# Optimization experiments

Measured on AMD Instinct MI355X. Metric: run time of the kernel, lower is better.

## Reference

```python
import jax, jax.numpy as jnp
import numpy as np

IN_SIZE = 1024
CLASSES = 7
N = 50000
LN_EPS = 1e-5


def _chain(x, w, b, g, beta):
    # Linear -> (Dropout=identity at eval) -> LayerNorm -> GELU(exact erf)
    h = x @ w.T + b
    mu = jnp.mean(h, axis=-1, keepdims=True)
    var = jnp.var(h, axis=-1, keepdims=True)
    h = (h - mu) / jnp.sqrt(var + LN_EPS) * g + beta
    return jax.nn.gelu(h, approximate=False)


def setup_inputs() -> dict:
    key = jax.random.key(0)
    ks = jax.random.split(key, 16)
    d = IN_SIZE
    std = 1.0 / np.sqrt(d)
    inp = {
        "features": jax.random.normal(ks[0], (N, d), jnp.float32),
        "c": jax.random.normal(ks[1], (N, CLASSES), jnp.float32),
        "key_w": jax.random.uniform(ks[2], (d, d), jnp.float32, -std, std),
        "key_b": jax.random.uniform(ks[3], (d,), jnp.float32, -std, std),
        "key_g": jnp.ones((d,), jnp.float32),
        "key_beta": jnp.zeros((d,), jnp.float32),
        "query_w": jax.random.uniform(ks[4], (d, d), jnp.float32, -std, std),
        "query_b": jax.random.uniform(ks[5], (d,), jnp.float32, -std, std),
        "query_g": jnp.ones((d,), jnp.float32),
        "query_beta": jnp.zeros((d,), jnp.float32),
        "value_w": jax.random.uniform(ks[6], (d, d), jnp.float32, -std, std),
        "value_b": jax.random.uniform(ks[7], (d,), jnp.float32, -std, std),
        "value_g": jnp.ones((d,), jnp.float32),
        "value_beta": jnp.zeros((d,), jnp.float32),
        "head_w": jax.random.uniform(ks[8], (CLASSES, CLASSES, d), jnp.float32, -1.0 / np.sqrt(CLASSES * d), 1.0 / np.sqrt(CLASSES * d)),
        "head_b": jax.random.uniform(ks[9], (CLASSES,), jnp.float32, -1.0 / np.sqrt(CLASSES * d), 1.0 / np.sqrt(CLASSES * d)),
    }
    return inp


def reference(features, c, key_w, key_b, key_g, key_beta,
              query_w, query_b, query_g, query_beta,
              value_w, value_b, value_g, value_beta,
              head_w, head_b):
    K = _chain(features, key_w, key_b, key_g, key_beta)          # [N, d]
    V = _chain(K, value_w, value_b, value_g, value_beta)         # [N, d]
    Q = _chain(K, query_w, query_b, query_g, query_beta)         # [N, d]
    # critical (top-scoring) instance per class
    top_idx = jnp.argmax(c, axis=0)                              # [classes]
    m_feats = K[top_idx]                                         # [classes, d]
    q_max = _chain(m_feats, query_w, query_b, query_g, query_beta)  # [classes, d]
    A = Q @ q_max.T                                              # [N, classes]
    A = jax.nn.softmax(A / jnp.sqrt(jnp.float32(Q.shape[1])), axis=0)
    B = A.T @ V                                                  # [classes, d]
    # Conv1d(classes, classes, kernel_size=d) on [1, classes, d] -> full contraction
    C = jnp.einsum('ik,oik->o', B, head_w) + head_b              # [classes]
    C = C.reshape(1, -1)
    return (C, A, B.reshape(1, CLASSES, -1))
```

## Files before the change

kernel.cpp:

```cpp
#include <hip/hip_runtime.h>


typedef unsigned short u16;
typedef __attribute__((ext_vector_type(8))) short          bf16x8;
typedef __attribute__((ext_vector_type(8))) unsigned short u16x8;
typedef __attribute__((ext_vector_type(4))) unsigned short u16x4;
typedef __attribute__((ext_vector_type(4))) float          f32x4;

#define DDIM  1024
#define NROWS 50000
#define MP    50048
#define NCLS  7
#define MPD4  12512

__device__ __forceinline__ u16 f2bf(float f) {
  unsigned u = __float_as_uint(f);
  u = (u + 0x7FFFu + ((u >> 16) & 1u)) >> 16;
  return (u16)u;
}
__device__ __forceinline__ float bf2f(u16 h) {
  return __uint_as_float(((unsigned)h) << 16);
}
__device__ __forceinline__ float gelu(float x) {
  return 0.5f * x * (1.0f + erff(x * 0.70710678118654752f));
}

__device__ __forceinline__ void load16_lds(const u16* g, u16* l) {
  __builtin_amdgcn_global_load_lds(
      (const __attribute__((address_space(1))) unsigned int*)(const void*)g,
      (__attribute__((address_space(3))) unsigned int*)(void*)l, 16, 0, 0);
}

__global__ __launch_bounds__(256) void k_convw(const float* __restrict__ kw,
                                               const float* __restrict__ vw,
                                               const float* __restrict__ qw,
                                               u16* __restrict__ Wk,
                                               u16* __restrict__ Wvq) {
  const int w = blockIdx.x >> 7;
  const int b = blockIdx.x & 127;
  const float* src = (w == 0) ? kw : (w == 1) ? vw : qw;
  u16* dst = (w == 0) ? Wk : (Wvq + (size_t)(w - 1) * DDIM * DDIM);
  for (int i = b * 256 + threadIdx.x; i < DDIM * DDIM / 8; i += 128 * 256) {
    const float4* p = (const float4*)(src + (size_t)i * 8);
    float4 f0 = p[0], f1 = p[1];
    u16x8 o;
    o[0] = f2bf(f0.x); o[1] = f2bf(f0.y); o[2] = f2bf(f0.z); o[3] = f2bf(f0.w);
    o[4] = f2bf(f1.x); o[5] = f2bf(f1.y); o[6] = f2bf(f1.z); o[7] = f2bf(f1.w);
    *(u16x8*)(dst + (size_t)i * 8) = o;
  }
}

template<int AFP32>
__global__ __launch_bounds__(256) void k_gemm(const float* __restrict__ Af,
                                              const u16* __restrict__ Ab,
                                              const u16* __restrict__ B,
                                              u16* __restrict__ C,
                                              int lnn, int ldc) {
  __shared__ __align__(16) u16 As[128 * 32];
  __shared__ __align__(16) u16 Bs[128 * 32];
  const int tid  = threadIdx.x;
  const int lane = tid & 63;
  const int cpx = gridDim.x >> 3;
  const int v   = (blockIdx.x & 7) * cpx + (blockIdx.x >> 3);
  const int m0 = (v >> lnn) * 128;
  const int n0 = (v & ((1 << lnn) - 1)) * 128;
  const int wid = tid >> 6;
  const int wr = (wid >> 1) * 64;
  const int wc = (wid & 1) * 64;

  const int rA = tid >> 2;
  const int slotl = tid & 3;
  const int swz = (rA >> 1) & 3;
  const int cA = ((slotl ^ swz) << 3);
  const u16* Bp0 = B + (size_t)(n0 + rA) * DDIM + cA;
  const u16* Bp1 = Bp0 + (size_t)64 * DDIM;
  const u16* Ap0 = nullptr; const u16* Ap1 = nullptr;
  const float* Fp0 = nullptr; const float* Fp1 = nullptr;
  bool av0 = false, av1 = false;
  if (AFP32) {
    av0 = (m0 + rA) < NROWS;
    av1 = (m0 + rA + 64) < NROWS;
    Fp0 = Af + (size_t)(m0 + rA) * DDIM + slotl * 8;
    Fp1 = Fp0 + (size_t)64 * DDIM;
  } else {
    Ap0 = Ab + (size_t)(m0 + rA) * DDIM + cA;
    Ap1 = Ap0 + (size_t)64 * DDIM;
  }
  const int wbase = wid * 64;
  u16* AsD0 = &As[(wbase)       * 8];
  u16* AsD1 = &As[(wbase + 256) * 8];
  u16* BsD0 = &Bs[(wbase)       * 8];
  u16* BsD1 = &Bs[(wbase + 256) * 8];
  u16* AsW0 = &As[rA * 32 + (cA ^ 0)];
  u16* AsW1 = &As[(rA + 64) * 32 + cA];

  f32x4 acc[4][4] = {};
  const int fr = lane & 15;
  const int T  = lane >> 4;

  for (int k0 = 0; k0 < DDIM; k0 += 32) {
    float4 fa0, fb0, fa1, fb1;
    if (AFP32) {
      if (av0) { fa0 = *(const float4*)(Fp0 + k0); fb0 = *(const float4*)(Fp0 + k0 + 4); }
      if (av1) { fa1 = *(const float4*)(Fp1 + k0); fb1 = *(const float4*)(Fp1 + k0 + 4); }
    }
    __syncthreads();
    if (AFP32) {
      u16x8 o0 = {0,0,0,0,0,0,0,0}, o1 = {0,0,0,0,0,0,0,0};
      if (av0) {
        o0[0]=f2bf(fa0.x); o0[1]=f2bf(fa0.y); o0[2]=f2bf(fa0.z); o0[3]=f2bf(fa0.w);
        o0[4]=f2bf(fb0.x); o0[5]=f2bf(fb0.y); o0[6]=f2bf(fb0.z); o0[7]=f2bf(fb0.w);
      }
      if (av1) {
        o1[0]=f2bf(fa1.x); o1[1]=f2bf(fa1.y); o1[2]=f2bf(fa1.z); o1[3]=f2bf(fa1.w);
        o1[4]=f2bf(fb1.x); o1[5]=f2bf(fb1.y); o1[6]=f2bf(fb1.z); o1[7]=f2bf(fb1.w);
      }
      *(u16x8*)AsW0 = o0;
      *(u16x8*)AsW1 = o1;
    } else {
      load16_lds(Ap0 + k0, AsD0);
      load16_lds(Ap1 + k0, AsD1);
    }
    load16_lds(Bp0 + k0, BsD0);
    load16_lds(Bp1 + k0, BsD1);
    __syncthreads();
    bf16x8 a[4], b[4];
#pragma unroll
    for (int i = 0; i < 4; ++i) {
      const int R = wr + i * 16 + fr;
      a[i] = *(const bf16x8*)&As[R * 32 + ((T ^ ((R >> 1) & 3)) << 3)];
    }
#pragma unroll
    for (int j = 0; j < 4; ++j) {
      const int R = wc + j * 16 + fr;
      b[j] = *(const bf16x8*)&Bs[R * 32 + ((T ^ ((R >> 1) & 3)) << 3)];
    }
#pragma unroll
    for (int i = 0; i < 4; ++i)
#pragma unroll
      for (int j = 0; j < 4; ++j)
        acc[i][j] = __builtin_amdgcn_mfma_f32_16x16x32_bf16(a[i], b[j], acc[i][j], 0, 0, 0);
  }

  const int orow = (lane >> 4) * 4;
  const int ocol = lane & 15;
#pragma unroll
  for (int i = 0; i < 4; ++i)
#pragma unroll
    for (int j = 0; j < 4; ++j) {
      const size_t base = (size_t)(m0 + wr + i * 16 + orow) * ldc + (n0 + wc + j * 16 + ocol);
#pragma unroll
      for (int r = 0; r < 4; ++r)
        C[base + (size_t)r * ldc] = f2bf(acc[i][j][r]);
    }
}

__global__ __launch_bounds__(256) void k_ln_k(const u16* __restrict__ h,
                                              const float* __restrict__ bias,
                                              const float* __restrict__ g,
                                              const float* __restrict__ beta,
                                              u16* __restrict__ out) {
  const int lane = threadIdx.x & 63;
  const int row = blockIdx.x * 4 + (threadIdx.x >> 6);
  const int c0 = lane * 8;
  u16x8* op0 = (u16x8*)(out + (size_t)row * DDIM + c0);
  u16x8* op1 = (u16x8*)(out + (size_t)row * DDIM + 512 + c0);
  if (row >= NROWS) {
    u16x8 z = {0, 0, 0, 0, 0, 0, 0, 0};
    *op0 = z; *op1 = z;
    return;
  }
  u16x8 h0 = *(const u16x8*)(h + (size_t)row * DDIM + c0);
  u16x8 h1 = *(const u16x8*)(h + (size_t)row * DDIM + 512 + c0);
  float4 a0 = *(const float4*)(bias + c0), a1 = *(const float4*)(bias + c0 + 4);
  float4 a2 = *(const float4*)(bias + 512 + c0), a3 = *(const float4*)(bias + 512 + c0 + 4);
  const float ba[8] = {a0.x, a0.y, a0.z, a0.w, a1.x, a1.y, a1.z, a1.w};
  const float bb[8] = {a2.x, a2.y, a2.z, a2.w, a3.x, a3.y, a3.z, a3.w};
  float v0[8], v1[8];
  float s1 = 0.f, s2 = 0.f;
#pragma unroll
  for (int e = 0; e < 8; ++e) {
    v0[e] = bf2f(h0[e]) + ba[e];
    v1[e] = bf2f(h1[e]) + bb[e];
    s1 += v0[e] + v1[e];
    s2 += v0[e] * v0[e] + v1[e] * v1[e];
  }
#pragma unroll
  for (int m = 1; m < 64; m <<= 1) {
    s1 += __shfl_xor(s1, m, 64);
    s2 += __shfl_xor(s2, m, 64);
  }
  const float mu = s1 * (1.0f / 1024.0f);
  const float var = s2 * (1.0f / 1024.0f) - mu * mu;
  const float rs = rsqrtf(var + 1e-5f);
  float4 g0 = *(const float4*)(g + c0), g1 = *(const float4*)(g + c0 + 4);
  float4 g2 = *(const float4*)(g + 512 + c0), g3 = *(const float4*)(g + 512 + c0 + 4);
  float4 t0 = *(const float4*)(beta + c0), t1 = *(const float4*)(beta + c0 + 4);
  float4 t2 = *(const float4*)(beta + 512 + c0), t3 = *(const float4*)(beta + 512 + c0 + 4);
  const float ga[8] = {g0.x, g0.y, g0.z, g0.w, g1.x, g1.y, g1.z, g1.w};
  const float gb[8] = {g2.x, g2.y, g2.z, g2.w, g3.x, g3.y, g3.z, g3.w};
  const float ta[8] = {t0.x, t0.y, t0.z, t0.w, t1.x, t1.y, t1.z, t1.w};
  const float tb[8] = {t2.x, t2.y, t2.z, t2.w, t3.x, t3.y, t3.z, t3.w};
  u16x8 o0, o1;
#pragma unroll
  for (int e = 0; e < 8; ++e) {
    o0[e] = f2bf(gelu((v0[e] - mu) * rs * ga[e] + ta[e]));
    o1[e] = f2bf(gelu((v1[e] - mu) * rs * gb[e] + tb[e]));
  }
  *op0 = o0; *op1 = o1;
}

__global__ __launch_bounds__(64) void k_qmax2(const float* __restrict__ argv,
                                              const int* __restrict__ argi,
                                              const u16* __restrict__ hvq,
                                              const float* __restrict__ qb,
                                              const float* __restrict__ qg,
                                              const float* __restrict__ qbeta,
                                              u16* __restrict__ qm) {
  const int j = blockIdx.x;
  const int lane = threadIdx.x;
  float bv = -3.4e38f; int bi = 0x7fffffff;
  for (int p = lane; p < 128; p += 64) {
    const float v = argv[p * NCLS + j];
    const int   i = argi[p * NCLS + j];
    if (v > bv || (v == bv && i < bi)) { bv = v; bi = i; }
  }
#pragma unroll
  for (int m = 1; m < 64; m <<= 1) {
    const float ov = __shfl_xor(bv, m, 64);
    const int   oi = __shfl_xor(bi, m, 64);
    if (ov > bv || (ov == bv && oi < bi)) { bv = ov; bi = oi; }
  }
  const int row = bi;
  const int c0 = lane * 8;
  const u16* hp = hvq + (size_t)row * 2048 + DDIM;
  u16x8 h0 = *(const u16x8*)(hp + c0);
  u16x8 h1 = *(const u16x8*)(hp + 512 + c0);
  float v0[8], v1[8];
  float s1 = 0.f, s2 = 0.f;
#pragma unroll
  for (int e = 0; e < 8; ++e) {
    v0[e] = bf2f(h0[e]) + qb[c0 + e];
    v1[e] = bf2f(h1[e]) + qb[512 + c0 + e];
    s1 += v0[e] + v1[e];
    s2 += v0[e] * v0[e] + v1[e] * v1[e];
  }
#pragma unroll
  for (int m = 1; m < 64; m <<= 1) {
    s1 += __shfl_xor(s1, m, 64);
    s2 += __shfl_xor(s2, m, 64);
  }
  const float mu = s1 * (1.0f / 1024.0f);
  const float var = s2 * (1.0f / 1024.0f) - mu * mu;
  const float rs = rsqrtf(var + 1e-5f);
  u16x8 o0, o1;
#pragma unroll
  for (int e = 0; e < 8; ++e) {
    o0[e] = f2bf(gelu((v0[e] - mu) * rs * qg[c0 + e] + qbeta[c0 + e]));
    o1[e] = f2bf(gelu((v1[e] - mu) * rs * qg[512 + c0 + e] + qbeta[512 + c0 + e]));
  }
  *(u16x8*)(qm + (size_t)j * DDIM + c0) = o0;
  *(u16x8*)(qm + (size_t)j * DDIM + 512 + c0) = o1;
}

__global__ __launch_bounds__(256) void k_ln_vq(const u16* __restrict__ h,
                                               const float* __restrict__ v_b,
                                               const float* __restrict__ v_g,
                                               const float* __restrict__ v_beta,
                                               const float* __restrict__ q_b,
                                               const float* __restrict__ q_g,
                                               const float* __restrict__ q_beta,
                                               const u16* __restrict__ qm,
                                               u16* __restrict__ V,
                                               float* __restrict__ logits) {
  __shared__ __align__(16) u16 sqm[NCLS * DDIM];
  const int tid = threadIdx.x;
  const int lane = tid & 63;
  const int half = (blockIdx.x >= MPD4) ? 1 : 0;
  const int rb = half ? (blockIdx.x - MPD4) : blockIdx.x;
  const int row = rb * 4 + (tid >> 6);
  if (half) {
    for (int i = tid; i < NCLS * DDIM / 8; i += 256)
      *(u16x8*)&sqm[i * 8] = *(const u16x8*)&qm[i * 8];
    __syncthreads();
  }
  if (row >= NROWS) return;
  const float* bias = half ? q_b : v_b;
  const float* gain = half ? q_g : v_g;
  const float* bet  = half ? q_beta : v_beta;
  const int c0 = lane * 8;
  const u16* hp = h + (size_t)row * 2048 + (size_t)half * DDIM;
  u16x8 h0 = *(const u16x8*)(hp + c0);
  u16x8 h1 = *(const u16x8*)(hp + 512 + c0);
  float4 a0 = *(const float4*)(bias + c0), a1 = *(const float4*)(bias + c0 + 4);
  float4 a2 = *(const float4*)(bias + 512 + c0), a3 = *(const float4*)(bias + 512 + c0 + 4);
  const float ba[8] = {a0.x, a0.y, a0.z, a0.w, a1.x, a1.y, a1.z, a1.w};
  const float bb[8] = {a2.x, a2.y, a2.z, a2.w, a3.x, a3.y, a3.z, a3.w};
  float v0[8], v1[8];
  float s1 = 0.f, s2 = 0.f;
#pragma unroll
  for (int e = 0; e < 8; ++e) {
    v0[e] = bf2f(h0[e]) + ba[e];
    v1[e] = bf2f(h1[e]) + bb[e];
    s1 += v0[e] + v1[e];
    s2 += v0[e] * v0[e] + v1[e] * v1[e];
  }
#pragma unroll
  for (int m = 1; m < 64; m <<= 1) {
    s1 += __shfl_xor(s1, m, 64);
    s2 += __shfl_xor(s2, m, 64);
  }
  const float mu = s1 * (1.0f / 1024.0f);
  const float var = s2 * (1.0f / 1024.0f) - mu * mu;
  const float rs = rsqrtf(var + 1e-5f);
  float4 g0 = *(const float4*)(gain + c0), g1 = *(const float4*)(gain + c0 + 4);
  float4 g2 = *(const float4*)(gain + 512 + c0), g3 = *(const float4*)(gain + 512 + c0 + 4);
  float4 t0 = *(const float4*)(bet + c0), t1 = *(const float4*)(bet + c0 + 4);
  float4 t2 = *(const float4*)(bet + 512 + c0), t3 = *(const float4*)(bet + 512 + c0 + 4);
  const float ga[8] = {g0.x, g0.y, g0.z, g0.w, g1.x, g1.y, g1.z, g1.w};
  const float gb[8] = {g2.x, g2.y, g2.z, g2.w, g3.x, g3.y, g3.z, g3.w};
  const float ta[8] = {t0.x, t0.y, t0.z, t0.w, t1.x, t1.y, t1.z, t1.w};
  const float tb[8] = {t2.x, t2.y, t2.z, t2.w, t3.x, t3.y, t3.z, t3.w};
  float y0[8], y1[8];
#pragma unroll
  for (int e = 0; e < 8; ++e) {
    y0[e] = gelu((v0[e] - mu) * rs * ga[e] + ta[e]);
    y1[e] = gelu((v1[e] - mu) * rs * gb[e] + tb[e]);
  }
  if (half == 0) {
    u16x8 o0, o1;
#pragma unroll
    for (int e = 0; e < 8; ++e) { o0[e] = f2bf(y0[e]); o1[e] = f2bf(y1[e]); }
    *(u16x8*)(V + (size_t)row * DDIM + c0) = o0;
    *(u16x8*)(V + (size_t)row * DDIM + 512 + c0) = o1;
  } else {
#pragma unroll
    for (int j = 0; j < NCLS; ++j) {
      u16x8 m0 = *(const u16x8*)&sqm[j * DDIM + c0];
      u16x8 m1 = *(const u16x8*)&sqm[j * DDIM + 512 + c0];
      float p = 0.f;
#pragma unroll
      for (int e = 0; e < 8; ++e) p += y0[e] * bf2f(m0[e]) + y1[e] * bf2f(m1[e]);
#pragma unroll
      for (int m = 1; m < 64; m <<= 1) p += __shfl_xor(p, m, 64);
      if (lane == 0) logits[(size_t)row * NCLS + j] = p * 0.03125f;
    }
  }
}

__global__ __launch_bounds__(256) void k_arg1(const float* __restrict__ c,
                                              float* __restrict__ pv,
                                              int* __restrict__ pi) {
  __shared__ float sv[256 * NCLS];
  __shared__ int   si[256 * NCLS];
  const int t = threadIdx.x;
  float bv[NCLS]; int bi[NCLS];
#pragma unroll
  for (int j = 0; j < NCLS; ++j) { bv[j] = -3.4e38f; bi[j] = 0x7fffffff; }
  for (int n = blockIdx.x * 256 + t; n < NROWS; n += 128 * 256) {
#pragma unroll
    for (int j = 0; j < NCLS; ++j) {
      const float v = c[(size_t)n * NCLS + j];
      if (v > bv[j]) { bv[j] = v; bi[j] = n; }
    }
  }
#pragma unroll
  for (int j = 0; j < NCLS; ++j) { sv[t * NCLS + j] = bv[j]; si[t * NCLS + j] = bi[j]; }
  __syncthreads();
  for (int s = 128; s > 0; s >>= 1) {
    if (t < s) {
#pragma unroll
      for (int j = 0; j < NCLS; ++j) {
        const float v2 = sv[(t + s) * NCLS + j]; const int i2 = si[(t + s) * NCLS + j];
        const float v1 = sv[t * NCLS + j];       const int i1 = si[t * NCLS + j];
        if (v2 > v1 || (v2 == v1 && i2 < i1)) { sv[t * NCLS + j] = v2; si[t * NCLS + j] = i2; }
      }
    }
    __syncthreads();
  }
  if (t < NCLS) { pv[blockIdx.x * NCLS + t] = sv[t]; pi[blockIdx.x * NCLS + t] = si[t]; }
}

__global__ __launch_bounds__(256) void k_softpart(const float* __restrict__ logits,
                                                  float* __restrict__ Pm,
                                                  float* __restrict__ Ps) {
  __shared__ float sm[256 * NCLS];
  const int t = threadIdx.x;
  float m[NCLS];
#pragma unroll
  for (int j = 0; j < NCLS; ++j) m[j] = -3.4e38f;
  for (int n = blockIdx.x * 256 + t; n < NROWS; n += 128 * 256)
#pragma unroll
    for (int j = 0; j < NCLS; ++j) m[j] = fmaxf(m[j], logits[(size_t)n * NCLS + j]);
#pragma unroll
  for (int j = 0; j < NCLS; ++j) sm[t * NCLS + j] = m[j];
  __syncthreads();
  for (int s = 128; s > 0; s >>= 1) {
    if (t < s)
#pragma unroll
      for (int j = 0; j < NCLS; ++j)
        sm[t * NCLS + j] = fmaxf(sm[t * NCLS + j], sm[(t + s) * NCLS + j]);
    __syncthreads();
  }
  float mloc[NCLS];
#pragma unroll
  for (int j = 0; j < NCLS; ++j) mloc[j] = sm[j];
  __syncthreads();
  float s[NCLS];
#pragma unroll
  for (int j = 0; j < NCLS; ++j) s[j] = 0.f;
  for (int n = blockIdx.x * 256 + t; n < NROWS; n += 128 * 256)
#pragma unroll
    for (int j = 0; j < NCLS; ++j) s[j] += expf(logits[(size_t)n * NCLS + j] - mloc[j]);
#pragma unroll
  for (int j = 0; j < NCLS; ++j) sm[t * NCLS + j] = s[j];
  __syncthreads();
  for (int st = 128; st > 0; st >>= 1) {
    if (t < st)
#pragma unroll
      for (int j = 0; j < NCLS; ++j) sm[t * NCLS + j] += sm[(t + st) * NCLS + j];
    __syncthreads();
  }
  if (t < NCLS) { Pm[blockIdx.x * NCLS + t] = mloc[t]; Ps[blockIdx.x * NCLS + t] = sm[t]; }
}

__global__ __launch_bounds__(256) void k_bpart(const float* __restrict__ logits,
                                               const float* __restrict__ Pm,
                                               const float* __restrict__ Ps,
                                               const u16* __restrict__ V,
                                               float* __restrict__ Aout,
                                               float* __restrict__ Pb) {
  __shared__ float sA[98 * NCLS];
  __shared__ float sM[NCLS], sR[NCLS];
  const int t = threadIdx.x;
  if (t < NCLS) {
    float M = -3.4e38f;
    for (int b = 0; b < 128; ++b) M = fmaxf(M, Pm[b * NCLS + t]);
    float S = 0.f;
    for (int b = 0; b < 128; ++b) S += Ps[b * NCLS + t] * expf(Pm[b * NCLS + t] - M);
    sM[t] = M; sR[t] = 1.0f / S;
  }
  __syncthreads();
  const int n0 = blockIdx.x * 98;
  int cnt = NROWS - n0;
  cnt = cnt < 0 ? 0 : (cnt > 98 ? 98 : cnt);
  for (int idx = t; idx < cnt * NCLS; idx += 256) {
    const int j = idx % NCLS;
    const float a = expf(logits[(size_t)n0 * NCLS + idx] - sM[j]) * sR[j];
    sA[idx] = a;
    Aout[(size_t)n0 * NCLS + idx] = a;
  }
  __syncthreads();
  float acc[NCLS][4] = {};
  for (int r = 0; r < cnt; ++r) {
    u16x4 vv = *(const u16x4*)&V[(size_t)(n0 + r) * DDIM + t * 4];
    const float f0 = bf2f(vv[0]), f1 = bf2f(vv[1]), f2 = bf2f(vv[2]), f3 = bf2f(vv[3]);
#pragma unroll
    for (int j = 0; j < NCLS; ++j) {
      const float a = sA[r * NCLS + j];
      acc[j][0] += a * f0; acc[j][1] += a * f1; acc[j][2] += a * f2; acc[j][3] += a * f3;
    }
  }
#pragma unroll
  for (int j = 0; j < NCLS; ++j) {
    f32x4 o = {acc[j][0], acc[j][1], acc[j][2], acc[j][3]};
    *(f32x4*)&Pb[((size_t)blockIdx.x * NCLS + j) * DDIM + t * 4] = o;
  }
}

__global__ void k_bred(const float* __restrict__ Pb, float* __restrict__ Bout) {
  const int idx = blockIdx.x * 256 + threadIdx.x;
  if (idx >= NCLS * DDIM) return;
  float s = 0.f;
  for (int p = 0; p < 512; ++p) s += Pb[(size_t)p * NCLS * DDIM + idx];
  Bout[idx] = s;
}

__global__ __launch_bounds__(256) void k_head(const float* __restrict__ Bmat,
                                              const float* __restrict__ hw,
                                              const float* __restrict__ hb,
                                              float* __restrict__ Cout) {
  const int o = blockIdx.x, t = threadIdx.x;
  float p = 0.f;
  for (int idx = t; idx < NCLS * DDIM; idx += 256)
    p += Bmat[idx] * hw[(size_t)o * NCLS * DDIM + idx];
#pragma unroll
  for (int m = 1; m < 64; m <<= 1) p += __shfl_xor(p, m, 64);
  __shared__ float w[4];
  if ((t & 63) == 0) w[t >> 6] = p;
  __syncthreads();
  if (t == 0) Cout[o] = w[0] + w[1] + w[2] + w[3] + hb[o];
}

extern "C" void kernel_launch(void* const* d_in, const int* in_sizes, int n_in,
                              void* d_out, int out_size, void* d_ws, size_t ws_size,
                              hipStream_t stream) {
  const float* features   = (const float*)d_in[0];
  const float* c_in       = (const float*)d_in[1];
  const float* key_w      = (const float*)d_in[2];
  const float* key_b      = (const float*)d_in[3];
  const float* key_g      = (const float*)d_in[4];
  const float* key_beta   = (const float*)d_in[5];
  const float* query_w    = (const float*)d_in[6];
  const float* query_b    = (const float*)d_in[7];
  const float* query_g    = (const float*)d_in[8];
  const float* query_beta = (const float*)d_in[9];
  const float* value_w    = (const float*)d_in[10];
  const float* value_b    = (const float*)d_in[11];
  const float* value_g    = (const float*)d_in[12];
  const float* value_beta = (const float*)d_in[13];
  const float* head_w     = (const float*)d_in[14];
  const float* head_b     = (const float*)d_in[15];

  char* ws = (char*)d_ws;
  const size_t SZB = (size_t)MP * DDIM * 2;
  u16* HbK  = (u16*)ws;
  u16* Kb   = (u16*)(ws + SZB);
  u16* HbVQ = (u16*)(ws + 2 * SZB);
  u16* Vb   = Kb;
  size_t off = 4 * SZB;
  u16* Wk  = (u16*)(ws + off); off += (size_t)DDIM * DDIM * 2;
  u16* Wvq = (u16*)(ws + off); off += (size_t)2 * DDIM * DDIM * 2;
  float* logits = (float*)(ws + off); off += ((size_t)NROWS * NCLS * 4 + 255) & ~(size_t)255;
  float* Pb  = (float*)(ws + off); off += (size_t)512 * NCLS * DDIM * 4;
  u16* qm    = (u16*)(ws + off); off += ((size_t)NCLS * DDIM * 2 + 255) & ~(size_t)255;
  float* Pmax = (float*)(ws + off); off += ((size_t)128 * NCLS * 4 + 255) & ~(size_t)255;
  float* Psum = (float*)(ws + off); off += ((size_t)128 * NCLS * 4 + 255) & ~(size_t)255;
  float* argv = (float*)(ws + off); off += ((size_t)128 * NCLS * 4 + 255) & ~(size_t)255;
  int*   argi = (int*)  (ws + off); off += ((size_t)128 * NCLS * 4 + 255) & ~(size_t)255;

  float* Cout = (float*)d_out;
  float* Aout = Cout + NCLS;
  float* Bout = Aout + (size_t)NROWS * NCLS;

  k_arg1<<<128, 256, 0, stream>>>(c_in, argv, argi);
  k_convw<<<384, 256, 0, stream>>>(key_w, value_w, query_w, Wk, Wvq);

  k_gemm<1><<<3128, 256, 0, stream>>>(features, nullptr, Wk, HbK, 3, 1024);
  k_ln_k<<<MPD4, 256, 0, stream>>>(HbK, key_b, key_g, key_beta, Kb);

  k_gemm<0><<<6256, 256, 0, stream>>>(nullptr, Kb, Wvq, HbVQ, 4, 2048);
  k_qmax2<<<NCLS, 64, 0, stream>>>(argv, argi, HbVQ, query_b, query_g, query_beta, qm);
  k_ln_vq<<<2 * MPD4, 256, 0, stream>>>(HbVQ, value_b, value_g, value_beta,
                                        query_b, query_g, query_beta, qm, Vb, logits);

  k_softpart<<<128, 256, 0, stream>>>(logits, Pmax, Psum);

  k_bpart<<<512, 256, 0, stream>>>(logits, Pmax, Psum, Vb, Aout, Pb);
  k_bred<<<28, 256, 0, stream>>>(Pb, Bout);
  k_head<<<NCLS, 256, 0, stream>>>(Bout, head_w, head_b, Cout);
}
```

Before: 746.2 us.

## Add 256x256-tile double-buffered GEMM kernel for the fused V/Q projection

Replaces the 128x128-tile GEMM for the combined value/query projection (N=2048) with a new 512-thread kernel using 256x256 tiles, 64-wide K steps and 128KB of double-buffered LDS filled via global_load_lds with XOR swizzling. It interleaves next-stage loads with MFMA phases, raises wave priority around MFMAs, and remaps blocks so neighbouring blocks share A/B tiles. Row padding grows to a multiple of 256, so the K-projection GEMM and LayerNorm grids grow slightly and buffers get larger. The intent is higher arithmetic intensity and less LDS/global traffic per MFMA, at the cost of heavy LDS use that limits occupancy and hand-placed barriers that are fragile.

```diff
diff --git a/kernel.cpp b/kernel.cpp
--- a/kernel.cpp
+++ b/kernel.cpp
@@ -9,9 +9,9 @@
 
 #define DDIM  1024
 #define NROWS 50000
-#define MP    50048
+#define MP    50176
 #define NCLS  7
-#define MPD4  12512
+#define MPD4  12544
 
 __device__ __forceinline__ u16 f2bf(float f) {
   unsigned u = __float_as_uint(f);
@@ -30,6 +30,8 @@
       (const __attribute__((address_space(1))) unsigned int*)(const void*)g,
       (__attribute__((address_space(3))) unsigned int*)(void*)l, 16, 0, 0);
 }
+
+#define MFMA_(a, b, c) __builtin_amdgcn_mfma_f32_16x16x32_bf16(a, b, c, 0, 0, 0)
 
 __global__ __launch_bounds__(256) void k_convw(const float* __restrict__ kw,
                                                const float* __restrict__ vw,
@@ -91,7 +93,7 @@
   u16* AsD1 = &As[(wbase + 256) * 8];
   u16* BsD0 = &Bs[(wbase)       * 8];
   u16* BsD1 = &Bs[(wbase + 256) * 8];
-  u16* AsW0 = &As[rA * 32 + (cA ^ 0)];
+  u16* AsW0 = &As[rA * 32 + cA];
   u16* AsW1 = &As[(rA + 64) * 32 + cA];
 
   f32x4 acc[4][4] = {};
@@ -139,7 +141,7 @@
     for (int i = 0; i < 4; ++i)
 #pragma unroll
       for (int j = 0; j < 4; ++j)
-        acc[i][j] = __builtin_amdgcn_mfma_f32_16x16x32_bf16(a[i], b[j], acc[i][j], 0, 0, 0);
+        acc[i][j] = MFMA_(a[i], b[j], acc[i][j]);
   }
 
   const int orow = (lane >> 4) * 4;
@@ -152,6 +154,111 @@
 #pragma unroll
       for (int r = 0; r < 4; ++r)
         C[base + (size_t)r * ldc] = f2bf(acc[i][j][r]);
+    }
+}
+
+__global__ __launch_bounds__(512, 2) void k_gemm256(const u16* __restrict__ A,
+                                                    const u16* __restrict__ Bw,
+                                                    u16* __restrict__ C) {
+  extern __shared__ __align__(16) u16 smem[];
+  u16* Abase = smem;
+  u16* Bbase = smem + 32768;
+  const int tid  = threadIdx.x;
+  const int lane = tid & 63;
+  const int wid  = tid >> 6;
+  const int wr = wid >> 2;
+  const int wc = wid & 3;
+  const int bh = wc >> 1;
+  const int bl = (wc & 1) * 64;
+  const int fr = lane & 15;
+  const int T  = lane >> 4;
+  const int v  = (blockIdx.x & 7) * 196 + (blockIdx.x >> 3);
+  const int m0 = (v >> 3) * 256;
+  const int n0 = (v & 7) * 256;
+
+  f32x4 acc[8][4] = {};
+
+#define STAGE_A(KT, BB) do {                                                   \
+    _Pragma("unroll") for (int h_ = 0; h_ < 2; ++h_)                           \
+      _Pragma("unroll") for (int l_ = 0; l_ < 2; ++l_) {                       \
+        const int s_ = l_ * 512 + tid;                                         \
+        const int r_ = s_ >> 3;                                                \
+        const int c_ = (s_ & 7) ^ (r_ & 7);                                    \
+        load16_lds(A + (size_t)(m0 + h_ * 128 + r_) * DDIM + (KT) * 64 + c_ * 8, \
+                   Abase + ((BB) * 2 + h_) * 8192 + s_ * 8);                   \
+      } } while (0)
+
+#define STAGE_B(KT, BB) do {                                                   \
+    _Pragma("unroll") for (int h_ = 0; h_ < 2; ++h_)                           \
+      _Pragma("unroll") for (int l_ = 0; l_ < 2; ++l_) {                       \
+        const int s_ = l_ * 512 + tid;                                         \
+        const int r_ = s_ >> 3;                                                \
+        const int c_ = (s_ & 7) ^ (r_ & 7);                                    \
+        load16_lds(Bw + (size_t)(n0 + h_ * 128 + r_) * DDIM + (KT) * 64 + c_ * 8, \
+                   Bbase + ((BB) * 2 + h_) * 8192 + s_ * 8);                   \
+      } } while (0)
+
+#define PHASE_A(p) do {                                                        \
+    bf16x8 afr[4];                                                             \
+    _Pragma("unroll") for (int ks = 0; ks < 2; ++ks)                           \
+      _Pragma("unroll") for (int ii = 0; ii < 2; ++ii) {                       \
+        const int R = ((p) * 2 + ii) * 16 + fr;                                \
+        afr[ks * 2 + ii] = *(const bf16x8*)&Ap[R * 64 + (((ks * 4 + T) ^ (R & 7)) << 3)]; \
+      }                                                                        \
+    __builtin_amdgcn_s_setprio(1);                                             \
+    _Pragma("unroll") for (int ks = 0; ks < 2; ++ks)                           \
+      _Pragma("unroll") for (int ii = 0; ii < 2; ++ii)                         \
+        _Pragma("unroll") for (int j = 0; j < 4; ++j)                          \
+          acc[(p) * 2 + ii][j] = MFMA_(afr[ks * 2 + ii], bfr[ks * 4 + j],      \
+                                       acc[(p) * 2 + ii][j]);                  \
+    __builtin_amdgcn_s_setprio(0);                                             \
+  } while (0)
+
+#define BARP() asm volatile("s_barrier" ::: "memory")
+
+  STAGE_A(0, 0);
+  STAGE_B(0, 0);
+  asm volatile("s_waitcnt vmcnt(0)\n\ts_barrier" ::: "memory");
+
+  for (int kt = 0; kt < 16; ++kt) {
+    const int b = kt & 1;
+    const u16* Ap = Abase + (b * 2 + wr) * 8192;
+    const u16* Bp = Bbase + (b * 2 + bh) * 8192;
+    const bool st = kt < 15;
+    bf16x8 bfr[8];
+    if (st) STAGE_A(kt + 1, b ^ 1);
+#pragma unroll
+    for (int ks = 0; ks < 2; ++ks)
+#pragma unroll
+      for (int j = 0; j < 4; ++j) {
+        const int R = bl + j * 16 + fr;
+        bfr[ks * 4 + j] = *(const bf16x8*)&Bp[R * 64 + (((ks * 4 + T) ^ (R & 7)) << 3)];
+      }
+    PHASE_A(0);
+    BARP();
+    if (st) STAGE_B(kt + 1, b ^ 1);
+    PHASE_A(1);
+    BARP();
+    PHASE_A(2);
+    BARP();
+    PHASE_A(3);
+    if (st)
+      asm volatile("s_waitcnt vmcnt(0) lgkmcnt(0)\n\ts_barrier" ::: "memory");
+  }
+#undef STAGE_A
+#undef STAGE_B
+#undef PHASE_A
+#undef BARP
+
+#pragma unroll
+  for (int i = 0; i < 8; ++i)
+#pragma unroll
+    for (int j = 0; j < 4; ++j) {
+      const size_t base = (size_t)(m0 + wr * 128 + i * 16 + T * 4) * 2048
+                        + (n0 + wc * 64 + j * 16 + fr);
+#pragma unroll
+      for (int r = 0; r < 4; ++r)
+        C[base + (size_t)r * 2048] = f2bf(acc[i][j][r]);
     }
 }
 
@@ -536,10 +643,10 @@
   k_arg1<<<128, 256, 0, stream>>>(c_in, argv, argi);
   k_convw<<<384, 256, 0, stream>>>(key_w, value_w, query_w, Wk, Wvq);
 
-  k_gemm<1><<<3128, 256, 0, stream>>>(features, nullptr, Wk, HbK, 3, 1024);
+  k_gemm<1><<<3136, 256, 0, stream>>>(features, nullptr, Wk, HbK, 3, 1024);
   k_ln_k<<<MPD4, 256, 0, stream>>>(HbK, key_b, key_g, key_beta, Kb);
 
-  k_gemm<0><<<6256, 256, 0, stream>>>(nullptr, Kb, Wvq, HbVQ, 4, 2048);
+  k_gemm256<<<1568, 512, 131072, stream>>>(Kb, Wvq, HbVQ);
   k_qmax2<<<NCLS, 64, 0, stream>>>(argv, argi, HbVQ, query_b, query_g, query_beta, qm);
   k_ln_vq<<<2 * MPD4, 256, 0, stream>>>(HbVQ, value_b, value_g, value_beta,
                                         query_b, query_g, query_beta, qm, Vb, logits);
```

Result: faster. 726.7 us, median of 2 (-2.6%).
